# Kernel optimization log

Measured on AMD Instinct MI355X. Metric: run time of the kernel, lower is better.

Reference implementation:

```python
import jax, jax.numpy as jnp
import numpy as np

EMBED_DIM = 1024
NUM_HEADS = 16
HEAD_DIM = EMBED_DIM // NUM_HEADS
CACHE_LEN = 16384


def setup_inputs() -> dict:
    key = jax.random.key(0)
    ks = jax.random.split(key, 10)
    s = 1.0 / np.sqrt(EMBED_DIM)
    return {
        "x": jax.random.normal(ks[0], (EMBED_DIM,), dtype=jnp.float32),
        "vk_cache": jax.random.normal(ks[1], (2, CACHE_LEN, NUM_HEADS, HEAD_DIM), dtype=jnp.float32),
        "Wv": jax.random.normal(ks[2], (EMBED_DIM, EMBED_DIM), dtype=jnp.float32) * s,
        "bv": jnp.zeros((EMBED_DIM,), dtype=jnp.float32),
        "Wq": jax.random.normal(ks[3], (EMBED_DIM, EMBED_DIM), dtype=jnp.float32) * s,
        "bq": jnp.zeros((EMBED_DIM,), dtype=jnp.float32),
        "Wk": jax.random.normal(ks[4], (EMBED_DIM, EMBED_DIM), dtype=jnp.float32) * s,
        "bk": jnp.zeros((EMBED_DIM,), dtype=jnp.float32),
        "Wo": jax.random.normal(ks[5], (EMBED_DIM, EMBED_DIM), dtype=jnp.float32) * s,
        "bo": jnp.zeros((EMBED_DIM,), dtype=jnp.float32),
    }


def reference(x, vk_cache, Wv, bv, Wq, bq, Wk, bk, Wo, bo):
    # Project single token to q/k/v
    v_i = (x @ Wv + bv).reshape(1, NUM_HEADS, HEAD_DIM)
    q_i = (x @ Wq + bq).reshape(NUM_HEADS, HEAD_DIM)
    k_i = (x @ Wk + bk).reshape(1, NUM_HEADS, HEAD_DIM)
    # Shift cache left by one, append new token   -> (CACHE_LEN, H, D)
    v = jnp.concatenate((vk_cache[0, 1:], v_i), axis=0)
    k = jnp.concatenate((vk_cache[1, 1:], k_i), axis=0)
    # Valid positions = any nonzero value entry
    mask = jnp.any(v != 0, axis=(1, 2))  # (CACHE_LEN,)
    # Scaled dot-product attention for the single query
    att = jnp.einsum('hd,khd->hk', q_i, k) / jnp.sqrt(jnp.float32(HEAD_DIM))
    att = jnp.where(mask, att, -jnp.inf)
    att = jax.nn.softmax(att, axis=-1)
    values = jnp.einsum('hk,khd->hd', att, v).reshape(EMBED_DIM)
    out_i = values @ Wo + bo
    return (out_i, jnp.stack([v, k]))
```

## Files before the change

### kernel.cpp

```cpp
#include <hip/hip_runtime.h>
#include <math.h>

#define EMBED 1024
#define NHEAD 16
#define HDIM  64
#define CLEN  16384

#define WS_QKV   0
#define WS_PM    3072
#define WS_PL    19456
#define WS_PACC  35840
#define WS_GM    1084416
#define WS_GL    1084928
#define WS_GACC  1085440
#define WS_VALS  1118208

__global__ __launch_bounds__(256) void qkv_proj(
    const float* __restrict__ x,
    const float* __restrict__ Wq, const float* __restrict__ bq,
    const float* __restrict__ Wk, const float* __restrict__ bk,
    const float* __restrict__ Wv, const float* __restrict__ bv,
    float* __restrict__ ws) {
  int m  = blockIdx.x >> 5;
  int i0 = (blockIdx.x & 31) * 32;
  const float* W; const float* b;
  if (m == 0)      { W = Wq; b = bq; }
  else if (m == 1) { W = Wk; b = bk; }
  else             { W = Wv; b = bv; }
  int j = threadIdx.x << 2;
  float4 acc = make_float4(0.f, 0.f, 0.f, 0.f);
  if (i0 == 0) acc = *(const float4*)(b + j);
  for (int i = i0; i < i0 + 32; ++i) {
    float xv = x[i];
    float4 w = *(const float4*)(W + (size_t)i * EMBED + j);
    acc.x += xv * w.x; acc.y += xv * w.y;
    acc.z += xv * w.z; acc.w += xv * w.w;
  }
  float* dst = ws + WS_QKV + (size_t)m * EMBED + j;
  atomicAdd(dst + 0, acc.x); atomicAdd(dst + 1, acc.y);
  atomicAdd(dst + 2, acc.z); atomicAdd(dst + 3, acc.w);
}

__global__ __launch_bounds__(256) void shift_attn(
    const float* __restrict__ cache,
    float* __restrict__ out,
    float* __restrict__ ws) {
  const int wave = ((blockIdx.x << 8) + threadIdx.x) >> 6;
  const int lane = threadIdx.x & 63;
  const int h    = lane >> 2;
  const int e    = h * HDIM + ((lane & 3) << 4);

  float qf[16];
#pragma unroll
  for (int j = 0; j < 16; j += 4) {
    float4 t = *(const float4*)(ws + WS_QKV + e + j);
    qf[j] = t.x; qf[j + 1] = t.y; qf[j + 2] = t.z; qf[j + 3] = t.w;
  }

  float mrun = -INFINITY, lsum = 0.f;
  float acc[16];
#pragma unroll
  for (int j = 0; j < 16; ++j) acc[j] = 0.f;

  const float* vin  = cache;
  const float* kin  = cache + (size_t)CLEN * EMBED;
  float* vout = out + EMBED;
  float* kout = out + EMBED + (size_t)CLEN * EMBED;
  const int t0 = wave * 16;

  for (int it = 0; it < 16; ++it) {
    int t = t0 + it;
    const float* vsrc = (t < CLEN - 1) ? (vin + (size_t)(t + 1) * EMBED + e)
                                       : (ws + WS_QKV + 2 * EMBED + e);
    const float* ksrc = (t < CLEN - 1) ? (kin + (size_t)(t + 1) * EMBED + e)
                                       : (ws + WS_QKV + EMBED + e);
    float vv[16], kk[16];
#pragma unroll
    for (int j = 0; j < 16; j += 4) {
      float4 tv = *(const float4*)(vsrc + j);
      vv[j] = tv.x; vv[j + 1] = tv.y; vv[j + 2] = tv.z; vv[j + 3] = tv.w;
    }
#pragma unroll
    for (int j = 0; j < 16; j += 4) {
      float4 tk = *(const float4*)(ksrc + j);
      kk[j] = tk.x; kk[j + 1] = tk.y; kk[j + 2] = tk.z; kk[j + 3] = tk.w;
    }
    float* vd = vout + (size_t)t * EMBED + e;
    float* kd = kout + (size_t)t * EMBED + e;
#pragma unroll
    for (int j = 0; j < 16; j += 4)
      *(float4*)(vd + j) = make_float4(vv[j], vv[j + 1], vv[j + 2], vv[j + 3]);
#pragma unroll
    for (int j = 0; j < 16; j += 4)
      *(float4*)(kd + j) = make_float4(kk[j], kk[j + 1], kk[j + 2], kk[j + 3]);

    bool nz = false;
#pragma unroll
    for (int j = 0; j < 16; ++j) nz = nz || (vv[j] != 0.f);
    float dot = 0.f;
#pragma unroll
    for (int j = 0; j < 16; ++j) dot += qf[j] * kk[j];
    dot += __shfl_xor(dot, 1, 64);
    dot += __shfl_xor(dot, 2, 64);

    if (__any((int)nz)) {
      float s  = dot * 0.125f;
      float mn = fmaxf(mrun, s);
      float alpha = __expf(mrun - mn);
      float p     = __expf(s - mn);
      lsum = lsum * alpha + p;
#pragma unroll
      for (int j = 0; j < 16; ++j) acc[j] = acc[j] * alpha + p * vv[j];
      mrun = mn;
    }
  }

  if ((lane & 3) == 0) {
    ws[WS_PM + wave * NHEAD + h] = mrun;
    ws[WS_PL + wave * NHEAD + h] = lsum;
  }
  float* pa = ws + WS_PACC + (size_t)wave * EMBED + e;
#pragma unroll
  for (int j = 0; j < 16; j += 4)
    *(float4*)(pa + j) = make_float4(acc[j], acc[j + 1], acc[j + 2], acc[j + 3]);
}

__global__ __launch_bounds__(1024) void combine1(float* __restrict__ ws) {
  int g = blockIdx.x;
  int tid = threadIdx.x;
  int h = tid >> 6;
  int w0 = g * 32;
  float M = -INFINITY;
  for (int w = w0; w < w0 + 32; ++w)
    M = fmaxf(M, ws[WS_PM + w * NHEAD + h]);
  float L = 0.f, a = 0.f;
  for (int w = w0; w < w0 + 32; ++w) {
    float sc = __expf(ws[WS_PM + w * NHEAD + h] - M);
    L += sc * ws[WS_PL + w * NHEAD + h];
    a += sc * ws[WS_PACC + (size_t)w * EMBED + tid];
  }
  if ((tid & 63) == 0) {
    ws[WS_GM + g * NHEAD + h] = M;
    ws[WS_GL + g * NHEAD + h] = L;
  }
  ws[WS_GACC + (size_t)g * EMBED + tid] = a;
}

__global__ __launch_bounds__(1024) void combine2(float* __restrict__ ws) {
  int tid = threadIdx.x;
  int h = tid >> 6;
  float M = -INFINITY;
  for (int g = 0; g < 32; ++g)
    M = fmaxf(M, ws[WS_GM + g * NHEAD + h]);
  float L = 0.f, a = 0.f;
  for (int g = 0; g < 32; ++g) {
    float sc = __expf(ws[WS_GM + g * NHEAD + h] - M);
    L += sc * ws[WS_GL + g * NHEAD + h];
    a += sc * ws[WS_GACC + (size_t)g * EMBED + tid];
  }
  ws[WS_VALS + tid] = a / L;
}

__global__ __launch_bounds__(256) void out_proj(
    const float* __restrict__ ws,
    const float* __restrict__ Wo, const float* __restrict__ bo,
    float* __restrict__ out) {
  int i0 = blockIdx.x * 32;
  int j = threadIdx.x << 2;
  float4 acc = make_float4(0.f, 0.f, 0.f, 0.f);
  if (i0 == 0) acc = *(const float4*)(bo + j);
  const float* vals = ws + WS_VALS;
  for (int i = i0; i < i0 + 32; ++i) {
    float xv = vals[i];
    float4 w = *(const float4*)(Wo + (size_t)i * EMBED + j);
    acc.x += xv * w.x; acc.y += xv * w.y;
    acc.z += xv * w.z; acc.w += xv * w.w;
  }
  atomicAdd(out + j + 0, acc.x); atomicAdd(out + j + 1, acc.y);
  atomicAdd(out + j + 2, acc.z); atomicAdd(out + j + 3, acc.w);
}

extern "C" void kernel_launch(void* const* d_in, const int* in_sizes, int n_in,
                              void* d_out, int out_size, void* d_ws, size_t ws_size,
                              hipStream_t stream) {
  const float* x     = (const float*)d_in[0];
  const float* cache = (const float*)d_in[1];
  const float* Wv    = (const float*)d_in[2];
  const float* bv    = (const float*)d_in[3];
  const float* Wq    = (const float*)d_in[4];
  const float* bq    = (const float*)d_in[5];
  const float* Wk    = (const float*)d_in[6];
  const float* bk    = (const float*)d_in[7];
  const float* Wo    = (const float*)d_in[8];
  const float* bo    = (const float*)d_in[9];
  float* out = (float*)d_out;
  float* ws  = (float*)d_ws;

  hipMemsetAsync(ws, 0, 3 * EMBED * sizeof(float), stream);
  hipMemsetAsync(out, 0, EMBED * sizeof(float), stream);

  qkv_proj  <<<96, 256, 0, stream>>>(x, Wq, bq, Wk, bk, Wv, bv, ws);
  shift_attn<<<256, 256, 0, stream>>>(cache, out, ws);
  combine1  <<<32, 1024, 0, stream>>>(ws);
  combine2  <<<1, 1024, 0, stream>>>(ws);
  out_proj  <<<32, 256, 0, stream>>>(ws, Wo, bo, out);
}
```

Measured before the change: 302.8 us.

## Spread shift-attention over more blocks and replace atomics with partial-sum reductions

The streaming shift/attention kernel now runs 1024 blocks, each covering 16 tokens split across its four waves. The waves merge their online-softmax state through shared memory, so the count of global partials stays the same. The intent is to put far more waves in flight for the memory-bound copy of the cache. The QKV and output projections now write per-chunk partials that small new reduce kernels sum with the biases, which removes the atomics and the two memsets. The cost is two extra kernel launches and more workspace traffic, and -inf guards were added to the merge steps.

```diff
diff --git a/kernel.cpp b/kernel.cpp
--- a/kernel.cpp
+++ b/kernel.cpp
@@ -7,45 +7,58 @@
 #define CLEN  16384
 
 #define WS_QKV   0
-#define WS_PM    3072
-#define WS_PL    19456
-#define WS_PACC  35840
-#define WS_GM    1084416
-#define WS_GL    1084928
-#define WS_GACC  1085440
-#define WS_VALS  1118208
+#define WS_QP    3072
+#define WS_PM    199680
+#define WS_PL    216064
+#define WS_PACC  232448
+#define WS_GM    1281024
+#define WS_GL    1281536
+#define WS_GACC  1282048
+#define WS_VALS  1314816
+#define WS_OPART 1315840
 
 __global__ __launch_bounds__(256) void qkv_proj(
     const float* __restrict__ x,
-    const float* __restrict__ Wq, const float* __restrict__ bq,
-    const float* __restrict__ Wk, const float* __restrict__ bk,
-    const float* __restrict__ Wv, const float* __restrict__ bv,
+    const float* __restrict__ Wq,
+    const float* __restrict__ Wk,
+    const float* __restrict__ Wv,
     float* __restrict__ ws) {
-  int m  = blockIdx.x >> 5;
-  int i0 = (blockIdx.x & 31) * 32;
-  const float* W; const float* b;
-  if (m == 0)      { W = Wq; b = bq; }
-  else if (m == 1) { W = Wk; b = bk; }
-  else             { W = Wv; b = bv; }
+  int m = blockIdx.x >> 6;
+  int c = blockIdx.x & 63;
+  const float* W = (m == 0) ? Wq : (m == 1) ? Wk : Wv;
   int j = threadIdx.x << 2;
+  int i0 = c * 16;
   float4 acc = make_float4(0.f, 0.f, 0.f, 0.f);
-  if (i0 == 0) acc = *(const float4*)(b + j);
-  for (int i = i0; i < i0 + 32; ++i) {
+  for (int i = i0; i < i0 + 16; ++i) {
     float xv = x[i];
     float4 w = *(const float4*)(W + (size_t)i * EMBED + j);
     acc.x += xv * w.x; acc.y += xv * w.y;
     acc.z += xv * w.z; acc.w += xv * w.w;
   }
-  float* dst = ws + WS_QKV + (size_t)m * EMBED + j;
-  atomicAdd(dst + 0, acc.x); atomicAdd(dst + 1, acc.y);
-  atomicAdd(dst + 2, acc.z); atomicAdd(dst + 3, acc.w);
+  *(float4*)(ws + WS_QP + (size_t)(m * 64 + c) * EMBED + j) = acc;
+}
+
+__global__ __launch_bounds__(256) void qkv_reduce(
+    const float* __restrict__ bq, const float* __restrict__ bk,
+    const float* __restrict__ bv, float* __restrict__ ws) {
+  int m = blockIdx.x >> 2;
+  int j = ((blockIdx.x & 3) << 8) + threadIdx.x;
+  const float* b = (m == 0) ? bq : (m == 1) ? bk : bv;
+  float s = b[j];
+  const float* p = ws + WS_QP + (size_t)m * 64 * EMBED + j;
+  for (int c = 0; c < 64; ++c) s += p[(size_t)c * EMBED];
+  ws[WS_QKV + m * EMBED + j] = s;
 }
 
 __global__ __launch_bounds__(256) void shift_attn(
     const float* __restrict__ cache,
     float* __restrict__ out,
     float* __restrict__ ws) {
-  const int wave = ((blockIdx.x << 8) + threadIdx.x) >> 6;
+  __shared__ float sacc[4][EMBED];
+  __shared__ float sm[4][NHEAD];
+  __shared__ float sl[4][NHEAD];
+
+  const int wv   = threadIdx.x >> 6;
   const int lane = threadIdx.x & 63;
   const int h    = lane >> 2;
   const int e    = h * HDIM + ((lane & 3) << 4);
@@ -62,13 +75,13 @@
 #pragma unroll
   for (int j = 0; j < 16; ++j) acc[j] = 0.f;
 
-  const float* vin  = cache;
-  const float* kin  = cache + (size_t)CLEN * EMBED;
+  const float* vin = cache;
+  const float* kin = cache + (size_t)CLEN * EMBED;
   float* vout = out + EMBED;
   float* kout = out + EMBED + (size_t)CLEN * EMBED;
-  const int t0 = wave * 16;
-
-  for (int it = 0; it < 16; ++it) {
+  const int t0 = blockIdx.x * 16 + wv * 4;
+
+  for (int it = 0; it < 4; ++it) {
     int t = t0 + it;
     const float* vsrc = (t < CLEN - 1) ? (vin + (size_t)(t + 1) * EMBED + e)
                                        : (ws + WS_QKV + 2 * EMBED + e);
@@ -115,69 +128,104 @@
     }
   }
 
-  if ((lane & 3) == 0) {
-    ws[WS_PM + wave * NHEAD + h] = mrun;
-    ws[WS_PL + wave * NHEAD + h] = lsum;
-  }
-  float* pa = ws + WS_PACC + (size_t)wave * EMBED + e;
-#pragma unroll
-  for (int j = 0; j < 16; j += 4)
-    *(float4*)(pa + j) = make_float4(acc[j], acc[j + 1], acc[j + 2], acc[j + 3]);
+  if (wv > 0) {
+#pragma unroll
+    for (int j = 0; j < 16; j += 4)
+      *(float4*)(&sacc[wv][e + j]) =
+          make_float4(acc[j], acc[j + 1], acc[j + 2], acc[j + 3]);
+    if ((lane & 3) == 0) { sm[wv][h] = mrun; sl[wv][h] = lsum; }
+  }
+  __syncthreads();
+  if (wv == 0) {
+    for (int w = 1; w < 4; ++w) {
+      float m2 = sm[w][h];
+      float M  = fmaxf(mrun, m2);
+      float a1 = (mrun == -INFINITY) ? 0.f : __expf(mrun - M);
+      float a2 = (m2   == -INFINITY) ? 0.f : __expf(m2 - M);
+      lsum = a1 * lsum + a2 * sl[w][h];
+#pragma unroll
+      for (int j = 0; j < 16; j += 4) {
+        float4 av = *(const float4*)(&sacc[w][e + j]);
+        acc[j]     = a1 * acc[j]     + a2 * av.x;
+        acc[j + 1] = a1 * acc[j + 1] + a2 * av.y;
+        acc[j + 2] = a1 * acc[j + 2] + a2 * av.z;
+        acc[j + 3] = a1 * acc[j + 3] + a2 * av.w;
+      }
+      mrun = M;
+    }
+    if ((lane & 3) == 0) {
+      ws[WS_PM + blockIdx.x * NHEAD + h] = mrun;
+      ws[WS_PL + blockIdx.x * NHEAD + h] = lsum;
+    }
+    float* pa = ws + WS_PACC + (size_t)blockIdx.x * EMBED + e;
+#pragma unroll
+    for (int j = 0; j < 16; j += 4)
+      *(float4*)(pa + j) =
+          make_float4(acc[j], acc[j + 1], acc[j + 2], acc[j + 3]);
+  }
 }
 
 __global__ __launch_bounds__(1024) void combine1(float* __restrict__ ws) {
-  int g = blockIdx.x;
-  int tid = threadIdx.x;
-  int h = tid >> 6;
+  int g = blockIdx.x, t = threadIdx.x, h = t >> 6;
   int w0 = g * 32;
   float M = -INFINITY;
   for (int w = w0; w < w0 + 32; ++w)
     M = fmaxf(M, ws[WS_PM + w * NHEAD + h]);
   float L = 0.f, a = 0.f;
   for (int w = w0; w < w0 + 32; ++w) {
-    float sc = __expf(ws[WS_PM + w * NHEAD + h] - M);
+    float mw = ws[WS_PM + w * NHEAD + h];
+    float sc = (mw == -INFINITY) ? 0.f : __expf(mw - M);
     L += sc * ws[WS_PL + w * NHEAD + h];
-    a += sc * ws[WS_PACC + (size_t)w * EMBED + tid];
-  }
-  if ((tid & 63) == 0) {
+    a += sc * ws[WS_PACC + (size_t)w * EMBED + t];
+  }
+  if ((t & 63) == 0) {
     ws[WS_GM + g * NHEAD + h] = M;
     ws[WS_GL + g * NHEAD + h] = L;
   }
-  ws[WS_GACC + (size_t)g * EMBED + tid] = a;
+  ws[WS_GACC + (size_t)g * EMBED + t] = a;
 }
 
 __global__ __launch_bounds__(1024) void combine2(float* __restrict__ ws) {
-  int tid = threadIdx.x;
-  int h = tid >> 6;
+  int t = threadIdx.x, h = t >> 6;
   float M = -INFINITY;
   for (int g = 0; g < 32; ++g)
     M = fmaxf(M, ws[WS_GM + g * NHEAD + h]);
   float L = 0.f, a = 0.f;
   for (int g = 0; g < 32; ++g) {
-    float sc = __expf(ws[WS_GM + g * NHEAD + h] - M);
+    float mg = ws[WS_GM + g * NHEAD + h];
+    float sc = (mg == -INFINITY) ? 0.f : __expf(mg - M);
     L += sc * ws[WS_GL + g * NHEAD + h];
-    a += sc * ws[WS_GACC + (size_t)g * EMBED + tid];
-  }
-  ws[WS_VALS + tid] = a / L;
+    a += sc * ws[WS_GACC + (size_t)g * EMBED + t];
+  }
+  ws[WS_VALS + t] = a / L;
 }
 
 __global__ __launch_bounds__(256) void out_proj(
-    const float* __restrict__ ws,
-    const float* __restrict__ Wo, const float* __restrict__ bo,
-    float* __restrict__ out) {
-  int i0 = blockIdx.x * 32;
+    const float* __restrict__ ws_in,
+    const float* __restrict__ Wo,
+    float* __restrict__ ws) {
+  int c = blockIdx.x;
   int j = threadIdx.x << 2;
+  int i0 = c * 16;
+  const float* vals = ws_in + WS_VALS;
   float4 acc = make_float4(0.f, 0.f, 0.f, 0.f);
-  if (i0 == 0) acc = *(const float4*)(bo + j);
-  const float* vals = ws + WS_VALS;
-  for (int i = i0; i < i0 + 32; ++i) {
+  for (int i = i0; i < i0 + 16; ++i) {
     float xv = vals[i];
     float4 w = *(const float4*)(Wo + (size_t)i * EMBED + j);
     acc.x += xv * w.x; acc.y += xv * w.y;
     acc.z += xv * w.z; acc.w += xv * w.w;
   }
-  atomicAdd(out + j + 0, acc.x); atomicAdd(out + j + 1, acc.y);
-  atomicAdd(out + j + 2, acc.z); atomicAdd(out + j + 3, acc.w);
+  *(float4*)(ws + WS_OPART + (size_t)c * EMBED + j) = acc;
+}
+
+__global__ __launch_bounds__(1024) void out_reduce(
+    const float* __restrict__ ws, const float* __restrict__ bo,
+    float* __restrict__ out) {
+  int t = threadIdx.x;
+  float s = bo[t];
+  const float* p = ws + WS_OPART + t;
+  for (int c = 0; c < 64; ++c) s += p[(size_t)c * EMBED];
+  out[t] = s;
 }
 
 extern "C" void kernel_launch(void* const* d_in, const int* in_sizes, int n_in,
@@ -196,12 +244,11 @@
   float* out = (float*)d_out;
   float* ws  = (float*)d_ws;
 
-  hipMemsetAsync(ws, 0, 3 * EMBED * sizeof(float), stream);
-  hipMemsetAsync(out, 0, EMBED * sizeof(float), stream);
-
-  qkv_proj  <<<96, 256, 0, stream>>>(x, Wq, bq, Wk, bk, Wv, bv, ws);
-  shift_attn<<<256, 256, 0, stream>>>(cache, out, ws);
+  qkv_proj  <<<192, 256, 0, stream>>>(x, Wq, Wk, Wv, ws);
+  qkv_reduce<<<12, 256, 0, stream>>>(bq, bk, bv, ws);
+  shift_attn<<<1024, 256, 0, stream>>>(cache, out, ws);
   combine1  <<<32, 1024, 0, stream>>>(ws);
   combine2  <<<1, 1024, 0, stream>>>(ws);
-  out_proj  <<<32, 256, 0, stream>>>(ws, Wo, bo, out);
-}
+  out_proj  <<<64, 256, 0, stream>>>(ws, Wo, ws);
+  out_reduce<<<1, 1024, 0, stream>>>(ws, bo, out);
+}
```

New measurement: 297.6 us. About the same (-1.7%).
